# Kernel optimization log

Hardware: AMD Instinct MI355X
Metric: run time of the kernel (lower is better)

## Reference

```python
import jax, jax.numpy as jnp
import numpy as np

N = 50000      # nodes
E = 600000     # edges (avg degree 12)
C = 128        # in/out channels
NF = 256       # SchNet num_filters (hardcoded in module)
EC = 64        # edge_channels (RBF expansion)


def ssp(x):
    # shifted softplus used by SchNet
    return jax.nn.softplus(x) - jnp.log(2.0).astype(x.dtype)


def setup_inputs() -> dict:
    key = jax.random.key(0)
    ks = jax.random.split(key, 16)
    def w(k, shape, fan_in):
        return jax.random.normal(k, shape, jnp.float32) * (1.0 / np.sqrt(fan_in))
    return {
        "x": jax.random.normal(ks[0], (N, C), jnp.float32),
        "edge_index": jax.random.randint(ks[1], (2, E), 0, N, jnp.int32),
        "edge_attr": jax.random.normal(ks[2], (E, EC), jnp.float32),
        "x_pos": jax.random.normal(ks[3], (N, 3), jnp.float32),
        # SchNet filter network: Linear(EC,NF) -> ssp -> Linear(NF,NF)
        "W_f1": w(ks[4], (EC, NF), EC), "b_f1": jnp.zeros((NF,), jnp.float32),
        "W_f2": w(ks[5], (NF, NF), NF), "b_f2": jnp.zeros((NF,), jnp.float32),
        # CFConv lin1 (no bias), lin2, then output lin3
        "W_lin1": w(ks[6], (C, NF), C),
        "W_lin2": w(ks[7], (NF, C), NF), "b_lin2": jnp.zeros((C,), jnp.float32),
        "W_lin3": w(ks[8], (C, C), C), "b_lin3": jnp.zeros((C,), jnp.float32),
        # edge MLP: Linear(EC + C, C) -> Tanh
        "W_e": w(ks[9], (EC + C, C), EC + C), "b_e": jnp.zeros((C,), jnp.float32),
    }


def reference(x, edge_index, edge_attr, x_pos,
              W_f1, b_f1, W_f2, b_f2,
              W_lin1, W_lin2, b_lin2, W_lin3, b_lin3,
              W_e, b_e):
    n = x.shape[0]
    row, col = edge_index[0], edge_index[1]

    # SchNet interaction (cfconv): edge filter net on edge_attr
    Wf = ssp(edge_attr @ W_f1 + b_f1) @ W_f2 + b_f2      # [E, NF]
    h = x @ W_lin1                                        # [N, NF]
    msg = h[col] * Wf                                     # [E, NF] gather + modulate
    agg = jax.ops.segment_sum(msg, row, num_segments=n)   # [N, NF] scatter-sum
    y = ssp(agg @ W_lin2 + b_lin2) @ W_lin3 + b_lin3      # [N, C]

    # relu + residual skip
    x_out = jax.nn.relu(y) + x

    # edge gather-MLP with residual on edge_attr
    e_in = jnp.concatenate([edge_attr, x_out[row] + x_out[col]], axis=-1)  # [E, EC+C]
    e_out = jnp.tanh(e_in @ W_e + b_e) + edge_attr if False else jnp.tanh(e_in @ W_e + b_e)
    # note: original adds residual only on edge_attr channels; shapes differ (C vs EC)
    # Linear maps to in_channels=C... but residual is `+ edge_attr` [E,EC]. In the repo
    # edge_channels == in_channels is required for this add; here EC != C, so we
    # follow the module math with EC projected: use the faithful form below.
    return x_out, e_out
```

## Files before the change

### kernel.cpp

```cpp
#include <hip/hip_runtime.h>

#define NN  50000
#define NE  600000
#define CC  128
#define NFF 256
#define ECH 64
#define EIN 192

typedef __attribute__((ext_vector_type(8))) short bf16x8;
typedef __attribute__((ext_vector_type(4))) short bf16x4;
typedef __attribute__((ext_vector_type(4))) float f32x4;
typedef __attribute__((ext_vector_type(4))) unsigned u32x4;
typedef __attribute__((ext_vector_type(2))) unsigned u32x2;

__device__ __forceinline__ float sspf(float v) {
    float e = __expf(-fabsf(v));
    return fmaxf(v, 0.f) + __logf(1.f + e) - 0.693147180559945f;
}
__device__ __forceinline__ float ftanh(float v) {
    float e = __expf(-2.f * fabsf(v));
    float r = (1.f - e) / (1.f + e);
    return copysignf(r, v);
}
__device__ __forceinline__ short bf16r(float f) {
    unsigned u = __float_as_uint(f);
    u = (u + 0x7FFFu + ((u >> 16) & 1u)) >> 16;
    return (short)u;
}
__device__ __forceinline__ unsigned cvtpk(float lo, float hi) {
    unsigned r;
    asm("v_cvt_pk_bf16_f32 %0, %1, %2" : "=v"(r) : "v"(lo), "v"(hi));
    return r;
}
__device__ __forceinline__ float bfu_lo(unsigned u) { return __uint_as_float(u << 16); }
__device__ __forceinline__ float bfu_hi(unsigned u) { return __uint_as_float(u & 0xffff0000u); }

#define PO_WF1 0
#define PO_WF2 16384
#define PO_WE  81920
#define PO_WL1 106496
#define PO_WL2 139264
#define PO_WL3 172032
#define P_TOT  188416
__global__ void kpack(const float* __restrict__ Wf1, const float* __restrict__ Wf2,
                      const float* __restrict__ We,  const float* __restrict__ Wl1,
                      const float* __restrict__ Wl2, const float* __restrict__ Wl3,
                      short* __restrict__ p) {
    int i = blockIdx.x * 256 + threadIdx.x;
    if (i < PO_WF2) {
        int t = i - PO_WF1;
        int j = t & 7, lane = (t >> 3) & 63, n16 = (t >> 9) & 15, ks = t >> 13;
        p[i] = bf16r(Wf1[(ks * 32 + (lane >> 4) * 8 + j) * NFF + n16 * 16 + (lane & 15)]);
    } else if (i < PO_WE) {
        int t = i - PO_WF2;
        int j = t & 7, lane = (t >> 3) & 63, n16 = (t >> 9) & 15, ks = t >> 13;
        int kp = ks * 32 + (lane >> 4) * 8 + j;
        int k = (kp >> 6) * 64 + (kp & 3) * 16 + ((kp >> 2) & 15);
        p[i] = bf16r(Wf2[k * NFF + n16 * 16 + (lane & 15)]);
    } else if (i < PO_WL1) {
        int t = i - PO_WE;
        int j = t & 7, lane = (t >> 3) & 63, n16 = (t >> 9) & 7, ks = t >> 12;
        p[i] = bf16r(We[(ks * 32 + (lane >> 4) * 8 + j) * CC + n16 * 16 + (lane & 15)]);
    } else if (i < PO_WL2) {
        int t = i - PO_WL1;
        int j = t & 7, lane = (t >> 3) & 63, n16 = (t >> 9) & 15, ks = t >> 13;
        p[i] = bf16r(Wl1[(ks * 32 + (lane >> 4) * 8 + j) * NFF + n16 * 16 + (lane & 15)]);
    } else if (i < PO_WL3) {
        int t = i - PO_WL2;
        int j = t & 7, lane = (t >> 3) & 63, n16 = (t >> 9) & 7, ks = t >> 12;
        int kp = ks * 32 + (lane >> 4) * 8 + j;
        int k = (kp >> 6) * 64 + (kp & 3) * 16 + ((kp >> 2) & 15);
        p[i] = bf16r(Wl2[k * CC + n16 * 16 + (lane & 15)]);
    } else if (i < P_TOT) {
        int t = i - PO_WL3;
        int j = t & 7, lane = (t >> 3) & 63, n16 = (t >> 9) & 7, ks = t >> 12;
        int kp = ks * 32 + (lane >> 4) * 8 + j;
        int k = (kp >> 5) * 32 + (kp & 1) * 16 + ((kp & 31) >> 1);
        p[i] = bf16r(Wl3[k * CC + n16 * 16 + (lane & 15)]);
    }
}

__global__ void k0_zero2(float* __restrict__ p0, long n40,
                         float* __restrict__ p1, long n41) {
    long i = (long)blockIdx.x * blockDim.x + threadIdx.x;
    long stride = (long)gridDim.x * blockDim.x;
    float4 z = {0.f, 0.f, 0.f, 0.f};
    for (long k = i; k < n40; k += stride) ((float4*)p0)[k] = z;
    for (long k = i; k < n41; k += stride) ((float4*)p1)[k] = z;
}

__global__ void k_cnt(const int* __restrict__ eidx, int* __restrict__ cnt) {
    int e = blockIdx.x * 256 + threadIdx.x;
    if (e < NE) atomicAdd(&cnt[eidx[e]], 1);
}

__global__ __launch_bounds__(256) void k_scan1(const int* __restrict__ cnt,
                                               int* __restrict__ offw,
                                               int* __restrict__ bsum) {
    __shared__ int sw_[4];
    int i = blockIdx.x * 256 + threadIdx.x;
    int lane = threadIdx.x & 63, wv = threadIdx.x >> 6;
    int v = (i < NN) ? cnt[i] : 0;
    int inc = v;
    #pragma unroll
    for (int d = 1; d < 64; d <<= 1) {
        int t = __shfl_up(inc, d, 64);
        if (lane >= d) inc += t;
    }
    if (lane == 63) sw_[wv] = inc;
    __syncthreads();
    int woff = 0;
    #pragma unroll
    for (int k = 0; k < 4; ++k) woff += (k < wv) ? sw_[k] : 0;
    if (i < NN) offw[i] = woff + inc - v;
    if (threadIdx.x == 255) bsum[blockIdx.x] = woff + inc;
}

__global__ __launch_bounds__(256) void k_scan2(int* __restrict__ bsum, int nb) {
    __shared__ int sw_[4];
    int t = threadIdx.x;
    int lane = t & 63, wv = t >> 6;
    int v = (t < nb) ? bsum[t] : 0;
    int inc = v;
    #pragma unroll
    for (int d = 1; d < 64; d <<= 1) {
        int s = __shfl_up(inc, d, 64);
        if (lane >= d) inc += s;
    }
    if (lane == 63) sw_[wv] = inc;
    __syncthreads();
    int woff = 0;
    #pragma unroll
    for (int k = 0; k < 4; ++k) woff += (k < wv) ? sw_[k] : 0;
    if (t < nb) bsum[t] = woff + inc - v;
}

__global__ void k_scan3(int* __restrict__ offw, const int* __restrict__ bsum,
                        int* __restrict__ rowptr) {
    int i = blockIdx.x * 256 + threadIdx.x;
    if (i < NN) {
        int v = offw[i] + bsum[blockIdx.x];
        offw[i] = v;
        rowptr[i] = v;
    }
    if (i == 0) rowptr[NN] = NE;
}

__global__ void k_scatter(const int* __restrict__ eidx, const float* __restrict__ ea,
                          int* __restrict__ offw, short* __restrict__ ea_s,
                          int* __restrict__ col_s, int* __restrict__ row_s) {
    int e = blockIdx.x * 256 + threadIdx.x;
    if (e >= NE) return;
    int r = eidx[e], c = eidx[NE + e];
    int pos = atomicAdd(&offw[r], 1);
    col_s[pos] = c;
    row_s[pos] = r;
    const float4* src = (const float4*)(ea + (size_t)e * ECH);
    short* dst = ea_s + (size_t)pos * ECH;
    #pragma unroll
    for (int i = 0; i < 4; ++i) {
        float4 f0 = src[4 * i], f1 = src[4 * i + 1], f2 = src[4 * i + 2], f3 = src[4 * i + 3];
        u32x4 v0 = {cvtpk(f0.x, f0.y), cvtpk(f0.z, f0.w), cvtpk(f1.x, f1.y), cvtpk(f1.z, f1.w)};
        u32x4 v1 = {cvtpk(f2.x, f2.y), cvtpk(f2.z, f2.w), cvtpk(f3.x, f3.y), cvtpk(f3.z, f3.w)};
        *(u32x4*)(dst + i * 16) = v0;
        *(u32x4*)(dst + i * 16 + 8) = v1;
    }
}

__global__ __launch_bounds__(256) void k1_h(const float* __restrict__ x,
                                            const short* __restrict__ pW,
                                            short* __restrict__ h) {
    __shared__ char xS[32 * 256];
    int n0 = blockIdx.x * 32;
    int tid = threadIdx.x;
    int lane = tid & 63, w = tid >> 6, q = lane >> 4, l15 = lane & 15;
    {
        int r = tid >> 3, seg = tid & 7;
        int rr = min(n0 + r, NN - 1);
        const float4* src = (const float4*)(x + (size_t)rr * CC + seg * 16);
        float4 f0 = src[0], f1 = src[1], f2 = src[2], f3 = src[3];
        u32x4 c0 = {cvtpk(f0.x, f0.y), cvtpk(f0.z, f0.w), cvtpk(f1.x, f1.y), cvtpk(f1.z, f1.w)};
        u32x4 c1 = {cvtpk(f2.x, f2.y), cvtpk(f2.z, f2.w), cvtpk(f3.x, f3.y), cvtpk(f3.z, f3.w)};
        int sw = (r & 7) << 4;
        *(u32x4*)(xS + r * 256 + ((seg * 32) ^ sw)) = c0;
        *(u32x4*)(xS + r * 256 + ((seg * 32 + 16) ^ sw)) = c1;
    }
    __syncthreads();

    f32x4 acc[2][4];
    #pragma unroll
    for (int mf = 0; mf < 2; ++mf)
        #pragma unroll
        for (int nf = 0; nf < 4; ++nf) acc[mf][nf] = f32x4{0.f, 0.f, 0.f, 0.f};

    #pragma unroll
    for (int ks = 0; ks < 4; ++ks) {
        bf16x8 a[2];
        #pragma unroll
        for (int mf = 0; mf < 2; ++mf) {
            int row = mf * 16 + l15;
            a[mf] = *(const bf16x8*)(xS + row * 256 + ((ks * 64 + q * 16) ^ ((row & 7) << 4)));
        }
        #pragma unroll
        for (int nf = 0; nf < 4; ++nf) {
            bf16x8 b = *(const bf16x8*)(pW + PO_WL1 + (((ks * 16 + w * 4 + nf) * 64) + lane) * 8);
            #pragma unroll
            for (int mf = 0; mf < 2; ++mf)
                acc[mf][nf] = __builtin_amdgcn_mfma_f32_16x16x32_bf16(a[mf], b, acc[mf][nf], 0, 0, 0);
        }
    }
    #pragma unroll
    for (int mf = 0; mf < 2; ++mf) {
        #pragma unroll
        for (int r = 0; r < 4; ++r) {
            int n = n0 + mf * 16 + q * 4 + r;
            if (n < NN) {
                u32x2 v = {cvtpk(acc[mf][0][r], acc[mf][1][r]),
                           cvtpk(acc[mf][2][r], acc[mf][3][r])};
                *(u32x2*)(h + (size_t)n * NFF + w * 64 + l15 * 4) = v;
            }
        }
    }
}

__global__ __launch_bounds__(256, 4) void k2b_agg(
        const short* __restrict__ ea_s, const int* __restrict__ col_s,
        const int* __restrict__ row_s,
        const short* __restrict__ pW, const float* __restrict__ bf1v,
        const float* __restrict__ bf2v,
        const short* __restrict__ h, float* __restrict__ agg) {
    __shared__ char t1S[64 * 512];
    __shared__ int colS[64], rowS[64];
    int s0 = blockIdx.x * 64;
    int tid = threadIdx.x;
    int lane = tid & 63, w = tid >> 6;
    int q = lane >> 4, l15 = lane & 15;

    if (tid < 64) {
        colS[tid] = col_s[s0 + tid];
        rowS[tid] = row_s[s0 + tid];
    }

    f32x4 acc[4][4];
    #pragma unroll
    for (int mf = 0; mf < 4; ++mf)
        #pragma unroll
        for (int nf = 0; nf < 4; ++nf) acc[mf][nf] = f32x4{0.f, 0.f, 0.f, 0.f};

    #pragma unroll
    for (int ks = 0; ks < 2; ++ks) {
        bf16x8 a[4];
        #pragma unroll
        for (int mf = 0; mf < 4; ++mf)
            a[mf] = *(const bf16x8*)(ea_s + (size_t)(s0 + mf * 16 + l15) * ECH + ks * 32 + q * 8);
        #pragma unroll
        for (int nf = 0; nf < 4; ++nf) {
            bf16x8 b = *(const bf16x8*)(pW + PO_WF1 + (((ks * 16 + w * 4 + nf) * 64) + lane) * 8);
            #pragma unroll
            for (int mf = 0; mf < 4; ++mf)
                acc[mf][nf] = __builtin_amdgcn_mfma_f32_16x16x32_bf16(a[mf], b, acc[mf][nf], 0, 0, 0);
        }
    }
    {
        float bia[4];
        #pragma unroll
        for (int nf = 0; nf < 4; ++nf) bia[nf] = bf1v[w * 64 + nf * 16 + l15];
        #pragma unroll
        for (int mf = 0; mf < 4; ++mf) {
            #pragma unroll
            for (int r = 0; r < 4; ++r) {
                int row = mf * 16 + q * 4 + r;
                u32x2 v = {cvtpk(sspf(acc[mf][0][r] + bia[0]), sspf(acc[mf][1][r] + bia[1])),
                           cvtpk(sspf(acc[mf][2][r] + bia[2]), sspf(acc[mf][3][r] + bia[3]))};
                *(u32x2*)(t1S + row * 512 + ((w * 128 + l15 * 8) ^ ((row & 7) << 4))) = v;
            }
        }
    }
    __syncthreads();

    #pragma unroll
    for (int mf = 0; mf < 4; ++mf)
        #pragma unroll
        for (int nf = 0; nf < 4; ++nf) acc[mf][nf] = f32x4{0.f, 0.f, 0.f, 0.f};

    for (int ks = 0; ks < 8; ++ks) {
        bf16x8 a[4];
        #pragma unroll
        for (int mf = 0; mf < 4; ++mf) {
            int row = mf * 16 + l15;
            a[mf] = *(const bf16x8*)(t1S + row * 512 + ((ks * 64 + q * 16) ^ ((row & 7) << 4)));
        }
        #pragma unroll
        for (int nf = 0; nf < 4; ++nf) {
            bf16x8 b = *(const bf16x8*)(pW + PO_WF2 + (((ks * 16 + w * 4 + nf) * 64) + lane) * 8);
            #pragma unroll
            for (int mf = 0; mf < 4; ++mf)
                acc[mf][nf] = __builtin_amdgcn_mfma_f32_16x16x32_bf16(a[mf], b, acc[mf][nf], 0, 0, 0);
        }
    }
    __syncthreads();

    {
        int r = tid >> 2, ch = tid & 3;
        const short* hp = h + (size_t)colS[r] * NFF;
        int sw = (r & 7) << 4;
        #pragma unroll
        for (int i = 0; i < 8; ++i) {
            int chunk = ch + i * 4;
            bf16x8 v = *(const bf16x8*)(hp + chunk * 8);
            *(bf16x8*)(t1S + r * 512 + ((chunk * 16) ^ sw)) = v;
        }
    }
    __syncthreads();

    {
        float bia[4];
        #pragma unroll
        for (int nf = 0; nf < 4; ++nf) bia[nf] = bf2v[w * 64 + nf * 16 + l15];
        #pragma unroll
        for (int mf = 0; mf < 4; ++mf) {
            #pragma unroll
            for (int r = 0; r < 4; ++r) {
                int eloc = mf * 16 + q * 4 + r;
                char* addr = t1S + eloc * 512 + ((w * 128 + l15 * 8) ^ ((eloc & 7) << 4));
                u32x2 hv = *(const u32x2*)addr;
                float m0 = bfu_lo(hv[0]) * (acc[mf][0][r] + bia[0]);
                float m1 = bfu_hi(hv[0]) * (acc[mf][1][r] + bia[1]);
                float m2 = bfu_lo(hv[1]) * (acc[mf][2][r] + bia[2]);
                float m3 = bfu_hi(hv[1]) * (acc[mf][3][r] + bia[3]);
                u32x2 out = {cvtpk(m0, m1), cvtpk(m2, m3)};
                *(u32x2*)addr = out;
            }
        }
    }
    __syncthreads();

    {
        int cp = tid & 127;
        int h0 = (tid >> 7) * 32;
        float a0 = 0.f, a1 = 0.f;
        int cur = rowS[h0];
        bool first = true;
        for (int e = h0; e < h0 + 32; ++e) {
            int rw = rowS[e];
            if (rw != cur) {
                float* dst = agg + (size_t)cur * NFF + cp * 2;
                if (first) { atomicAdd(dst, a0); atomicAdd(dst + 1, a1); first = false; }
                else       { dst[0] = a0; dst[1] = a1; }
                a0 = 0.f; a1 = 0.f;
                cur = rw;
            }
            unsigned v = *(const unsigned*)(t1S + e * 512 + ((cp * 4) ^ ((e & 7) << 4)));
            a0 += bfu_lo(v);
            a1 += bfu_hi(v);
        }
        float* dst = agg + (size_t)cur * NFF + cp * 2;
        atomicAdd(dst, a0); atomicAdd(dst + 1, a1);
    }
}

__global__ __launch_bounds__(256) void k3_node(
        const float* __restrict__ agg,
        const short* __restrict__ pW, const float* __restrict__ bl2,
        const float* __restrict__ bl3,
        const float* __restrict__ x, float* __restrict__ xo) {
    __shared__ char aggS[32 * 512];
    __shared__ char t2S[32 * 256];
    int n0 = blockIdx.x * 32;
    int tid = threadIdx.x;
    int lane = tid & 63, w = tid >> 6, q = lane >> 4, l15 = lane & 15;

    {
        int nd = tid >> 3, c0 = (tid & 7) * 32;
        int n = n0 + nd;
        float a[32];
        if (n < NN) {
            const float4* src = (const float4*)(agg + (size_t)n * NFF + c0);
            #pragma unroll
            for (int j = 0; j < 8; ++j) {
                float4 v = src[j];
                a[4 * j] = v.x; a[4 * j + 1] = v.y; a[4 * j + 2] = v.z; a[4 * j + 3] = v.w;
            }
        } else {
            #pragma unroll
            for (int i = 0; i < 32; ++i) a[i] = 0.f;
        }
        int sw = (nd & 7) << 4;
        #pragma unroll
        for (int j = 0; j < 4; ++j) {
            u32x4 v = {cvtpk(a[j * 8 + 0], a[j * 8 + 1]), cvtpk(a[j * 8 + 2], a[j * 8 + 3]),
                       cvtpk(a[j * 8 + 4], a[j * 8 + 5]), cvtpk(a[j * 8 + 6], a[j * 8 + 7])};
            *(u32x4*)(aggS + nd * 512 + (((c0 + j * 8) * 2) ^ sw)) = v;
        }
    }
    __syncthreads();

    f32x4 acc[2][2];
    #pragma unroll
    for (int mf = 0; mf < 2; ++mf)
        #pragma unroll
        for (int nf = 0; nf < 2; ++nf) acc[mf][nf] = f32x4{0.f, 0.f, 0.f, 0.f};
    for (int ks = 0; ks < 8; ++ks) {
        bf16x8 a[2];
        #pragma unroll
        for (int mf = 0; mf < 2; ++mf) {
            int row = mf * 16 + l15;
            a[mf] = *(const bf16x8*)(aggS + row * 512 + ((ks * 64 + q * 16) ^ ((row & 7) << 4)));
        }
        #pragma unroll
        for (int nf = 0; nf < 2; ++nf) {
            bf16x8 b = *(const bf16x8*)(pW + PO_WL2 + (((ks * 8 + w * 2 + nf) * 64) + lane) * 8);
            #pragma unroll
            for (int mf = 0; mf < 2; ++mf)
                acc[mf][nf] = __builtin_amdgcn_mfma_f32_16x16x32_bf16(a[mf], b, acc[mf][nf], 0, 0, 0);
        }
    }
    {
        float bia[2];
        #pragma unroll
        for (int nf = 0; nf < 2; ++nf) bia[nf] = bl2[w * 32 + nf * 16 + l15];
        #pragma unroll
        for (int mf = 0; mf < 2; ++mf) {
            #pragma unroll
            for (int r = 0; r < 4; ++r) {
                int row = mf * 16 + q * 4 + r;
                unsigned u = cvtpk(sspf(acc[mf][0][r] + bia[0]), sspf(acc[mf][1][r] + bia[1]));
                *(unsigned*)(t2S + row * 256 + ((w * 64 + l15 * 4) ^ ((row & 7) << 4))) = u;
            }
        }
    }
    __syncthreads();

    f32x4 acc2[2][2];
    #pragma unroll
    for (int mf = 0; mf < 2; ++mf)
        #pragma unroll
        for (int nf = 0; nf < 2; ++nf) acc2[mf][nf] = f32x4{0.f, 0.f, 0.f, 0.f};
    #pragma unroll
    for (int ks = 0; ks < 4; ++ks) {
        bf16x8 a[2];
        #pragma unroll
        for (int mf = 0; mf < 2; ++mf) {
            int row = mf * 16 + l15;
            a[mf] = *(const bf16x8*)(t2S + row * 256 + ((ks * 64 + q * 16) ^ ((row & 7) << 4)));
        }
        #pragma unroll
        for (int nf = 0; nf < 2; ++nf) {
            bf16x8 b = *(const bf16x8*)(pW + PO_WL3 + (((ks * 8 + w * 2 + nf) * 64) + lane) * 8);
            #pragma unroll
            for (int mf = 0; mf < 2; ++mf)
                acc2[mf][nf] = __builtin_amdgcn_mfma_f32_16x16x32_bf16(a[mf], b, acc2[mf][nf], 0, 0, 0);
        }
    }
    #pragma unroll
    for (int nf = 0; nf < 2; ++nf) {
        int col = w * 32 + nf * 16 + l15;
        float bias = bl3[col];
        #pragma unroll
        for (int mf = 0; mf < 2; ++mf) {
            #pragma unroll
            for (int r = 0; r < 4; ++r) {
                int n = n0 + mf * 16 + q * 4 + r;
                if (n < NN) {
                    size_t o = (size_t)n * CC + col;
                    xo[o] = fmaxf(acc2[mf][nf][r] + bias, 0.f) + x[o];
                }
            }
        }
    }
}

__global__ __launch_bounds__(256) void k4_mfma(
        const float* __restrict__ ea, const int* __restrict__ eidx,
        const float* __restrict__ xo, const short* __restrict__ pW,
        const float* __restrict__ bev, float* __restrict__ eo) {
    __shared__ char aS[64 * 384];
    int e0 = blockIdx.x * 64;
    int tid = threadIdx.x;
    int lane = tid & 63, w = tid >> 6;
    int q = lane >> 4, l15 = lane & 15;

    {
        int r = tid >> 2, cp = tid & 3;
        const float4* src = (const float4*)(ea + (size_t)(e0 + r) * ECH + cp * 16);
        float4 f0 = src[0], f1 = src[1], f2 = src[2], f3 = src[3];
        u32x4 c0 = {cvtpk(f0.x, f0.y), cvtpk(f0.z, f0.w), cvtpk(f1.x, f1.y), cvtpk(f1.z, f1.w)};
        u32x4 c1 = {cvtpk(f2.x, f2.y), cvtpk(f2.z, f2.w), cvtpk(f3.x, f3.y), cvtpk(f3.z, f3.w)};
        int sw = (r & 7) << 4;
        *(u32x4*)(aS + r * 384 + ((cp * 32) ^ sw)) = c0;
        *(u32x4*)(aS + r * 384 + ((cp * 32 + 16) ^ sw)) = c1;
    }
    {
        int e = tid >> 2, p = tid & 3;
        int rr = eidx[e0 + e], cc = eidx[NE + e0 + e];
        const float4* xr = (const float4*)(xo + (size_t)rr * CC);
        const float4* xc = (const float4*)(xo + (size_t)cc * CC);
        int sw = (e & 7) << 4;
        #pragma unroll
        for (int it = 0; it < 8; ++it) {
            int fi = p + it * 4;
            float4 va = xr[fi], vb = xc[fi];
            u32x2 hv = {cvtpk(va.x + vb.x, va.y + vb.y), cvtpk(va.z + vb.z, va.w + vb.w)};
            int byte = (ECH + fi * 4) * 2;
            *(u32x2*)(aS + e * 384 + (byte ^ sw)) = hv;
        }
    }
    __syncthreads();

    f32x4 acc[8];
    #pragma unroll
    for (int nf = 0; nf < 8; ++nf) acc[nf] = f32x4{0.f, 0.f, 0.f, 0.f};

    #pragma unroll
    for (int ks = 0; ks < 6; ++ks) {
        int row = w * 16 + l15;
        bf16x8 a = *(const bf16x8*)(aS + row * 384 + ((ks * 64 + q * 16) ^ ((row & 7) << 4)));
        #pragma unroll
        for (int nf = 0; nf < 8; ++nf) {
            bf16x8 b = *(const bf16x8*)(pW + PO_WE + (((ks * 8 + nf) * 64) + lane) * 8);
            acc[nf] = __builtin_amdgcn_mfma_f32_16x16x32_bf16(a, b, acc[nf], 0, 0, 0);
        }
    }
    #pragma unroll
    for (int nf = 0; nf < 8; ++nf) {
        int col = nf * 16 + l15;
        float bias = bev[col];
        #pragma unroll
        for (int r = 0; r < 4; ++r) {
            int e = e0 + w * 16 + q * 4 + r;
            eo[(size_t)e * CC + col] = ftanh(acc[nf][r] + bias);
        }
    }
}

extern "C" void kernel_launch(void* const* d_in, const int* in_sizes, int n_in,
                              void* d_out, int out_size, void* d_ws, size_t ws_size,
                              hipStream_t stream) {
    const float* x   = (const float*)d_in[0];
    const int*   ei  = (const int*)d_in[1];
    const float* ea  = (const float*)d_in[2];
    const float* Wf1 = (const float*)d_in[4];
    const float* bf1 = (const float*)d_in[5];
    const float* Wf2 = (const float*)d_in[6];
    const float* bf2 = (const float*)d_in[7];
    const float* Wl1 = (const float*)d_in[8];
    const float* Wl2 = (const float*)d_in[9];
    const float* bl2 = (const float*)d_in[10];
    const float* Wl3 = (const float*)d_in[11];
    const float* bl3 = (const float*)d_in[12];
    const float* We  = (const float*)d_in[13];
    const float* be  = (const float*)d_in[14];

    float* xo = (float*)d_out;
    float* eo = xo + (size_t)NN * CC;

    short* h    = (short*)xo;
    char*  top  = (char*)d_out + (size_t)out_size * sizeof(float);
    short* ea_s = (short*)(top - (size_t)NE * ECH * 2);
    int*   col_s = (int*)((char*)ea_s - (size_t)NE * 4);
    int*   row_s = (int*)((char*)col_s - (size_t)NE * 4);
    float* agg  = (float*)((char*)row_s - (size_t)NN * NFF * 4);

    short* pW    = (short*)d_ws;
    int* cnt     = (int*)((char*)d_ws + 393216);
    int* offw    = cnt + NN;
    int* rowptr  = offw + NN;
    int* bsum    = rowptr + NN + 1;

    const int NB = (NN + 255) / 256;

    kpack<<<P_TOT / 256, 256, 0, stream>>>(Wf1, Wf2, We, Wl1, Wl2, Wl3, pW);
    k0_zero2<<<1024, 256, 0, stream>>>(agg, (long)NN * NFF / 4, (float*)cnt, NN / 4);
    k_cnt<<<(NE + 255) / 256, 256, 0, stream>>>(ei, cnt);
    k_scan1<<<NB, 256, 0, stream>>>(cnt, offw, bsum);
    k_scan2<<<1, 256, 0, stream>>>(bsum, NB);
    k_scan3<<<NB, 256, 0, stream>>>(offw, bsum, rowptr);
    k_scatter<<<(NE + 255) / 256, 256, 0, stream>>>(ei, ea, offw, ea_s, col_s, row_s);
    k1_h<<<(NN + 31) / 32, 256, 0, stream>>>(x, pW, h);
    k2b_agg<<<NE / 64, 256, 0, stream>>>(ea_s, col_s, row_s, pW, bf1, bf2, h, agg);
    k3_node<<<(NN + 31) / 32, 256, 0, stream>>>(agg, pW, bl2, bl3, x, xo);
    k4_mfma<<<NE / 64, 256, 0, stream>>>(ea, ei, xo, pW, be, eo);
}
```

Before: 525.5 us.

## Replace sorted edge_attr copy with permutation gather and fuse h gather into reduction

The scatter kernel no longer writes a bf16 copy of edge_attr in sorted order; it records a permutation, and the aggregation kernel gathers fp32 edge_attr rows through it and converts them to bf16 in registers. The separate staging of h[col] rows into shared memory and the in-place modulation pass are removed. The filter output is now stored to shared memory unmodulated, and the segment-reduction loop reads h directly from global memory and applies it with an FMA. This cuts a full write and read of the sorted edge_attr buffer plus one barrier phase. In exchange, edge_attr reads become non-coalesced random gathers, and each h access becomes a 4-byte global load inside the reduction loop.

```diff
diff --git a/kernel.cpp b/kernel.cpp
--- a/kernel.cpp
+++ b/kernel.cpp
@@ -8,7 +8,6 @@
 #define EIN 192
 
 typedef __attribute__((ext_vector_type(8))) short bf16x8;
-typedef __attribute__((ext_vector_type(4))) short bf16x4;
 typedef __attribute__((ext_vector_type(4))) float f32x4;
 typedef __attribute__((ext_vector_type(4))) unsigned u32x4;
 typedef __attribute__((ext_vector_type(2))) unsigned u32x2;
@@ -34,6 +33,8 @@
 }
 __device__ __forceinline__ float bfu_lo(unsigned u) { return __uint_as_float(u << 16); }
 __device__ __forceinline__ float bfu_hi(unsigned u) { return __uint_as_float(u & 0xffff0000u); }
+
+union cvu { u32x4 u; bf16x8 b; };
 
 #define PO_WF1 0
 #define PO_WF2 16384
@@ -146,25 +147,16 @@
     if (i == 0) rowptr[NN] = NE;
 }
 
-__global__ void k_scatter(const int* __restrict__ eidx, const float* __restrict__ ea,
-                          int* __restrict__ offw, short* __restrict__ ea_s,
-                          int* __restrict__ col_s, int* __restrict__ row_s) {
+__global__ void k_scatter(const int* __restrict__ eidx, int* __restrict__ offw,
+                          int* __restrict__ perm, int* __restrict__ col_s,
+                          int* __restrict__ row_s) {
     int e = blockIdx.x * 256 + threadIdx.x;
     if (e >= NE) return;
     int r = eidx[e], c = eidx[NE + e];
     int pos = atomicAdd(&offw[r], 1);
+    perm[pos] = e;
     col_s[pos] = c;
     row_s[pos] = r;
-    const float4* src = (const float4*)(ea + (size_t)e * ECH);
-    short* dst = ea_s + (size_t)pos * ECH;
-    #pragma unroll
-    for (int i = 0; i < 4; ++i) {
-        float4 f0 = src[4 * i], f1 = src[4 * i + 1], f2 = src[4 * i + 2], f3 = src[4 * i + 3];
-        u32x4 v0 = {cvtpk(f0.x, f0.y), cvtpk(f0.z, f0.w), cvtpk(f1.x, f1.y), cvtpk(f1.z, f1.w)};
-        u32x4 v1 = {cvtpk(f2.x, f2.y), cvtpk(f2.z, f2.w), cvtpk(f3.x, f3.y), cvtpk(f3.z, f3.w)};
-        *(u32x4*)(dst + i * 16) = v0;
-        *(u32x4*)(dst + i * 16 + 8) = v1;
-    }
 }
 
 __global__ __launch_bounds__(256) void k1_h(const float* __restrict__ x,
@@ -224,8 +216,8 @@
 }
 
 __global__ __launch_bounds__(256, 4) void k2b_agg(
-        const short* __restrict__ ea_s, const int* __restrict__ col_s,
-        const int* __restrict__ row_s,
+        const float* __restrict__ ea, const int* __restrict__ perm,
+        const int* __restrict__ col_s, const int* __restrict__ row_s,
         const short* __restrict__ pW, const float* __restrict__ bf1v,
         const float* __restrict__ bf2v,
         const short* __restrict__ h, float* __restrict__ agg) {
@@ -241,6 +233,10 @@
         rowS[tid] = row_s[s0 + tid];
     }
 
+    int eRow[4];
+    #pragma unroll
+    for (int mf = 0; mf < 4; ++mf) eRow[mf] = perm[s0 + mf * 16 + l15];
+
     f32x4 acc[4][4];
     #pragma unroll
     for (int mf = 0; mf < 4; ++mf)
@@ -251,8 +247,14 @@
     for (int ks = 0; ks < 2; ++ks) {
         bf16x8 a[4];
         #pragma unroll
-        for (int mf = 0; mf < 4; ++mf)
-            a[mf] = *(const bf16x8*)(ea_s + (size_t)(s0 + mf * 16 + l15) * ECH + ks * 32 + q * 8);
+        for (int mf = 0; mf < 4; ++mf) {
+            const float4* src = (const float4*)(ea + (size_t)eRow[mf] * ECH + ks * 32 + q * 8);
+            float4 f0 = src[0], f1 = src[1];
+            cvu cv;
+            cv.u = u32x4{cvtpk(f0.x, f0.y), cvtpk(f0.z, f0.w),
+                         cvtpk(f1.x, f1.y), cvtpk(f1.z, f1.w)};
+            a[mf] = cv.b;
+        }
         #pragma unroll
         for (int nf = 0; nf < 4; ++nf) {
             bf16x8 b = *(const bf16x8*)(pW + PO_WF1 + (((ks * 16 + w * 4 + nf) * 64) + lane) * 8);
@@ -301,19 +303,6 @@
     __syncthreads();
 
     {
-        int r = tid >> 2, ch = tid & 3;
-        const short* hp = h + (size_t)colS[r] * NFF;
-        int sw = (r & 7) << 4;
-        #pragma unroll
-        for (int i = 0; i < 8; ++i) {
-            int chunk = ch + i * 4;
-            bf16x8 v = *(const bf16x8*)(hp + chunk * 8);
-            *(bf16x8*)(t1S + r * 512 + ((chunk * 16) ^ sw)) = v;
-        }
-    }
-    __syncthreads();
-
-    {
         float bia[4];
         #pragma unroll
         for (int nf = 0; nf < 4; ++nf) bia[nf] = bf2v[w * 64 + nf * 16 + l15];
@@ -321,15 +310,10 @@
         for (int mf = 0; mf < 4; ++mf) {
             #pragma unroll
             for (int r = 0; r < 4; ++r) {
-                int eloc = mf * 16 + q * 4 + r;
-                char* addr = t1S + eloc * 512 + ((w * 128 + l15 * 8) ^ ((eloc & 7) << 4));
-                u32x2 hv = *(const u32x2*)addr;
-                float m0 = bfu_lo(hv[0]) * (acc[mf][0][r] + bia[0]);
-                float m1 = bfu_hi(hv[0]) * (acc[mf][1][r] + bia[1]);
-                float m2 = bfu_lo(hv[1]) * (acc[mf][2][r] + bia[2]);
-                float m3 = bfu_hi(hv[1]) * (acc[mf][3][r] + bia[3]);
-                u32x2 out = {cvtpk(m0, m1), cvtpk(m2, m3)};
-                *(u32x2*)addr = out;
+                int row = mf * 16 + q * 4 + r;
+                u32x2 v = {cvtpk(acc[mf][0][r] + bia[0], acc[mf][1][r] + bia[1]),
+                           cvtpk(acc[mf][2][r] + bia[2], acc[mf][3][r] + bia[3])};
+                *(u32x2*)(t1S + row * 512 + ((w * 128 + l15 * 8) ^ ((row & 7) << 4))) = v;
             }
         }
     }
@@ -337,11 +321,12 @@
 
     {
         int cp = tid & 127;
-        int h0 = (tid >> 7) * 32;
+        int h0w = (tid >> 7) * 32;
         float a0 = 0.f, a1 = 0.f;
-        int cur = rowS[h0];
+        int cur = rowS[h0w];
         bool first = true;
-        for (int e = h0; e < h0 + 32; ++e) {
+        #pragma unroll 8
+        for (int e = h0w; e < h0w + 32; ++e) {
             int rw = rowS[e];
             if (rw != cur) {
                 float* dst = agg + (size_t)cur * NFF + cp * 2;
@@ -350,9 +335,10 @@
                 a0 = 0.f; a1 = 0.f;
                 cur = rw;
             }
-            unsigned v = *(const unsigned*)(t1S + e * 512 + ((cp * 4) ^ ((e & 7) << 4)));
-            a0 += bfu_lo(v);
-            a1 += bfu_hi(v);
+            unsigned wf = *(const unsigned*)(t1S + e * 512 + ((cp * 4) ^ ((e & 7) << 4)));
+            unsigned hv = *(const unsigned*)(h + (size_t)colS[e] * NFF + cp * 2);
+            a0 = fmaf(bfu_lo(hv), bfu_lo(wf), a0);
+            a1 = fmaf(bfu_hi(hv), bfu_hi(wf), a1);
         }
         float* dst = agg + (size_t)cur * NFF + cp * 2;
         atomicAdd(dst, a0); atomicAdd(dst + 1, a1);
@@ -554,12 +540,12 @@
     float* xo = (float*)d_out;
     float* eo = xo + (size_t)NN * CC;
 
-    short* h    = (short*)xo;
-    char*  top  = (char*)d_out + (size_t)out_size * sizeof(float);
-    short* ea_s = (short*)(top - (size_t)NE * ECH * 2);
-    int*   col_s = (int*)((char*)ea_s - (size_t)NE * 4);
+    short* h     = (short*)xo;
+    char*  top   = (char*)d_out + (size_t)out_size * sizeof(float);
+    int*   perm  = (int*)(top - (size_t)NE * 4);
+    int*   col_s = (int*)((char*)perm - (size_t)NE * 4);
     int*   row_s = (int*)((char*)col_s - (size_t)NE * 4);
-    float* agg  = (float*)((char*)row_s - (size_t)NN * NFF * 4);
+    float* agg   = (float*)((char*)row_s - (size_t)NN * NFF * 4);
 
     short* pW    = (short*)d_ws;
     int* cnt     = (int*)((char*)d_ws + 393216);
@@ -575,9 +561,9 @@
     k_scan1<<<NB, 256, 0, stream>>>(cnt, offw, bsum);
     k_scan2<<<1, 256, 0, stream>>>(bsum, NB);
     k_scan3<<<NB, 256, 0, stream>>>(offw, bsum, rowptr);
-    k_scatter<<<(NE + 255) / 256, 256, 0, stream>>>(ei, ea, offw, ea_s, col_s, row_s);
+    k_scatter<<<(NE + 255) / 256, 256, 0, stream>>>(ei, offw, perm, col_s, row_s);
     k1_h<<<(NN + 31) / 32, 256, 0, stream>>>(x, pW, h);
-    k2b_agg<<<NE / 64, 256, 0, stream>>>(ea_s, col_s, row_s, pW, bf1, bf2, h, agg);
+    k2b_agg<<<NE / 64, 256, 0, stream>>>(ea, perm, col_s, row_s, pW, bf1, bf2, h, agg);
     k3_node<<<(NN + 31) / 32, 256, 0, stream>>>(agg, pW, bl2, bl3, x, xo);
     k4_mfma<<<NE / 64, 256, 0, stream>>>(ea, ei, xo, pW, be, eo);
 }
```

Measured after the change: 580.7 us. +10.5%, slower.
